# Kernel tuning notes

Hardware: AMD Instinct MI355X
Metric: run time of the kernel (lower is better)

Reference implementation:

```python
import jax, jax.numpy as jnp
import numpy as np

B, T, D, R = 8, 4096, 768, 16
DB = D // 3  # bucket size (d_img = d_sym = 256, d_rf = D - 2*DB = 256)


def setup_inputs() -> dict:
    key = jax.random.key(0)
    ks = jax.random.split(key, 10)
    s = 0.05
    x = jax.random.normal(ks[0], (B, T, D), dtype=jnp.float32)
    # torch nn.Linear stores weight as (out, in); y = x @ W.T + b
    V_w = jax.random.normal(ks[1], (R, D), dtype=jnp.float32) * s
    U_w = jax.random.normal(ks[2], (D, R), dtype=jnp.float32) * s
    E1_w = jax.random.normal(ks[3], (DB, D), dtype=jnp.float32) * s
    E1_b = jnp.zeros((DB,), dtype=jnp.float32)
    E2_w = jax.random.normal(ks[4], (3, DB), dtype=jnp.float32) * s
    E2_b = jnp.zeros((3,), dtype=jnp.float32)
    # a_base init per bucket: img=-0.6, sym=-1.0, rf=-1.6; a_delta init 0 (perturbed so tanh path is exercised)
    a_base = jnp.concatenate([
        jnp.full((DB,), -0.6, dtype=jnp.float32),
        jnp.full((DB,), -1.0, dtype=jnp.float32),
        jnp.full((D - 2 * DB,), -1.6, dtype=jnp.float32),
    ])
    a_delta = jax.random.normal(ks[5], (D,), dtype=jnp.float32) * 0.1
    C_w = jax.random.normal(ks[6], (D, D), dtype=jnp.float32) * s
    G_w = jax.random.normal(ks[7], (D, D), dtype=jnp.float32) * s
    G_b = jnp.zeros((D,), dtype=jnp.float32)
    return {"x": x, "V_w": V_w, "U_w": U_w, "E1_w": E1_w, "E1_b": E1_b,
            "E2_w": E2_w, "E2_b": E2_b, "a_base": a_base, "a_delta": a_delta,
            "C_w": C_w, "G_w": G_w, "G_b": G_b}


def reference(x, V_w, U_w, E1_w, E1_b, E2_w, E2_b, a_base, a_delta, C_w, G_w, G_b):
    d = x.shape[-1]
    db = d // 3
    # Low-rank input projection: Bu = U(V(x))
    Z = jnp.einsum('btd,rd->btr', x, V_w)            # (B,T,R)
    Bu = jnp.einsum('btr,dr->btd', Z, U_w)           # (B,T,D)
    # Evidence scores per timestep (3 clinical buckets)
    h = jax.nn.gelu(jnp.einsum('btd,ed->bte', x, E1_w) + E1_b, approximate=False)
    alpha = jax.nn.sigmoid(jnp.einsum('bte,ce->btc', h, E2_w) + E2_b)  # (B,T,3)
    # Broadcast each bucket's evidence score over its channels
    alpha_rep = jnp.concatenate([
        jnp.broadcast_to(alpha[..., 0:1], alpha.shape[:-1] + (db,)),
        jnp.broadcast_to(alpha[..., 1:2], alpha.shape[:-1] + (db,)),
        jnp.broadcast_to(alpha[..., 2:3], alpha.shape[:-1] + (d - 2 * db,)),
    ], axis=-1)                                       # (B,T,D)
    a_eff = a_base + alpha_rep * jnp.tanh(a_delta)    # (B,T,D)
    lam = jnp.exp(-jax.nn.softplus(-a_eff))           # (B,T,D), in (0,1)
    # Diagonal linear recurrence s_t = lam_t * s_{t-1} + Bu_t  (scan over time)
    def step(s, inp):
        l_t, bu_t = inp
        s = l_t * s + bu_t
        return s, s
    s0 = jnp.zeros(x.shape[:1] + x.shape[2:], dtype=x.dtype)  # (B,D)
    _, S = jax.lax.scan(step, s0, (jnp.swapaxes(lam, 0, 1), jnp.swapaxes(Bu, 0, 1)))
    S = jnp.swapaxes(S, 0, 1)                         # (B,T,D)
    y = jnp.einsum('btd,od->bto', S, C_w)
    gate = jax.nn.sigmoid(jnp.einsum('btd,od->bto', x, G_w) + G_b)
    y = jax.nn.gelu(y, approximate=False) * gate
    return x + y  # dropout is identity in eval mode
```

## Files before the change

kernel.cpp:

```cpp
#include <hip/hip_runtime.h>
#include <hip/hip_bf16.h>
#include <math.h>

#define B_   8
#define T_   4096
#define D_   768
#define R_   16
#define DB_  256
#define N_   (B_ * T_)
#define NC_  64
#define L_   (T_ / NC_)
#define NKS_ (D_ / 32)
#define BUF_ 12288

typedef __attribute__((ext_vector_type(8))) short bf16x8;
typedef __attribute__((ext_vector_type(4))) float f32x4;

__device__ __forceinline__ float gelu_exact(float x) {
    return 0.5f * x * (1.0f + erff(x * 0.70710678118654752f));
}
__device__ __forceinline__ float sigmoidf_(float x) {
    return 1.0f / (1.0f + expf(-x));
}
__device__ __forceinline__ float bf2f(unsigned short u) {
    return __uint_as_float(((unsigned)u) << 16);
}
__device__ __forceinline__ unsigned short f2bf(float f) {
    __hip_bfloat16 h = __float2bfloat16(f);
    return *(unsigned short*)&h;
}
__device__ __forceinline__ bf16x8 pack8(float4 a, float4 b) {
    bf16x8 r;
    r[0] = (short)f2bf(a.x); r[1] = (short)f2bf(a.y);
    r[2] = (short)f2bf(a.z); r[3] = (short)f2bf(a.w);
    r[4] = (short)f2bf(b.x); r[5] = (short)f2bf(b.y);
    r[6] = (short)f2bf(b.z); r[7] = (short)f2bf(b.w);
    return r;
}

__device__ __forceinline__ void gload16(const unsigned short* g, unsigned short* l) {
    __builtin_amdgcn_global_load_lds(
        (const __attribute__((address_space(1))) unsigned int*)(const void*)g,
        (__attribute__((address_space(3))) unsigned int*)(void*)l,
        16, 0, 0);
}

__device__ __forceinline__ void stage_a(const unsigned short* src, int row0, int k0,
                                        unsigned short* lds, int w, int l) {
#pragma unroll
    for (int j = 0; j < 2; ++j) {
        int i   = ((w * 2 + j) << 6) + l;
        int row = i >> 2;
        int q   = i & 3;
        int qs  = q ^ ((row >> 1) & 3);
        gload16(src + (size_t)(row0 + row) * D_ + k0 + qs * 8, lds + ((w * 2 + j) << 9));
    }
}
__device__ __forceinline__ void stage_b(const unsigned short* src, int col0, int k0,
                                        unsigned short* lds, int w, int l) {
    int i   = (w << 6) + l;
    int row = i >> 2;
    int q   = i & 3;
    int qs  = q ^ ((row >> 1) & 3);
    gload16(src + (size_t)(col0 + row) * D_ + k0 + qs * 8, lds + (w << 9));
}

__device__ __forceinline__ bf16x8 frag_read(const unsigned short* lds, int row, int lq) {
    int q = lq ^ ((row >> 1) & 3);
    return *(const bf16x8*)(lds + row * 32 + q * 8);
}

__device__ __forceinline__ void tile_mfma(const unsigned short* la, const unsigned short* lb,
                                          int wrow, int wcol, int lr, int lq,
                                          f32x4 acc[4][4]) {
    bf16x8 a[4], b[4];
#pragma unroll
    for (int m = 0; m < 4; m++) a[m] = frag_read(la, wrow + m * 16 + lr, lq);
#pragma unroll
    for (int n = 0; n < 4; n++) b[n] = frag_read(lb, wcol + n * 16 + lr, lq);
    __builtin_amdgcn_s_setprio(1);
#pragma unroll
    for (int m = 0; m < 4; m++)
#pragma unroll
        for (int n = 0; n < 4; n++)
            acc[m][n] = __builtin_amdgcn_mfma_f32_16x16x32_bf16(a[m], b[n], acc[m][n], 0, 0, 0);
    __builtin_amdgcn_s_setprio(0);
}

__device__ __forceinline__ void kloop_prologue(const unsigned short* __restrict__ A,
                                               const unsigned short* __restrict__ Bm,
                                               int row0, int col0,
                                               unsigned short* lds, int w, int l) {
    stage_a(A, row0, 0,  lds,                w, l);
    stage_b(Bm, col0, 0,  lds + 8192,        w, l);
    stage_a(A, row0, 32, lds + BUF_,         w, l);
    stage_b(Bm, col0, 32, lds + BUF_ + 8192, w, l);
}

template <bool DO_PROLOGUE>
__device__ __forceinline__ void kloop3(const unsigned short* __restrict__ A,
                                       const unsigned short* __restrict__ Bm,
                                       int row0, int col0,
                                       unsigned short* lds,
                                       int w, int l, f32x4 acc[4][4]) {
    const int lr = l & 15, lq = l >> 4;
    const int wrow = (w >> 1) * 64, wcol = (w & 1) * 64;

    if (DO_PROLOGUE) kloop_prologue(A, Bm, row0, col0, lds, w, l);

#pragma unroll 3
    for (int t = 0; t < NKS_ - 2; ++t) {
        asm volatile("s_waitcnt vmcnt(3)" ::: "memory");
        __builtin_amdgcn_s_barrier();
        __builtin_amdgcn_sched_barrier(0);
        unsigned short* bn = lds + ((t + 2) % 3) * BUF_;
        stage_a(A, row0, (t + 2) * 32, bn,        w, l);
        stage_b(Bm, col0, (t + 2) * 32, bn + 8192, w, l);
        unsigned short* bc = lds + (t % 3) * BUF_;
        tile_mfma(bc, bc + 8192, wrow, wcol, lr, lq, acc);
    }
    asm volatile("s_waitcnt vmcnt(3)" ::: "memory");
    __builtin_amdgcn_s_barrier();
    __builtin_amdgcn_sched_barrier(0);
    {
        unsigned short* bc = lds + ((NKS_ - 2) % 3) * BUF_;
        tile_mfma(bc, bc + 8192, wrow, wcol, lr, lq, acc);
    }
    asm volatile("s_waitcnt vmcnt(0)" ::: "memory");
    __builtin_amdgcn_s_barrier();
    __builtin_amdgcn_sched_barrier(0);
    {
        unsigned short* bc = lds + ((NKS_ - 1) % 3) * BUF_;
        tile_mfma(bc, bc + 8192, wrow, wcol, lr, lq, acc);
    }
}

__device__ __forceinline__ void tile_decode(int nwg, int ncol, int& rowt, int& colt) {
    int bid = blockIdx.x;
    int cpx = nwg >> 3;
    int swz = (bid & 7) * cpx + (bid >> 3);
    colt = swz % ncol;
    rowt = swz / ncol;
}

__global__ __launch_bounds__(512, 2)
void gemm_e1_alpha(const unsigned short* __restrict__ Xb,
                   const unsigned short* __restrict__ Wb,
                   const float* __restrict__ bias,
                   const float* __restrict__ E2w,
                   float* __restrict__ alpha_acc) {
    __shared__ unsigned short lds[3 * BUF_];
    const int t = threadIdx.x, l = t & 63, w = t >> 6;
    int rowt, colt;
    tile_decode(256, 2, rowt, colt);
    const int row0 = rowt * 256, col0 = colt * 128;
    const int lr = l & 15, lq = l >> 4;
    const int wrow = (w >> 1) * 64, wcol = (w & 1) * 64;
    f32x4 acc[4][4] = {};
    kloop3<true>(Xb, Wb, row0, col0, lds, w, l, acc);

    float bia[4], e2v[3][4];
#pragma unroll
    for (int n = 0; n < 4; n++) {
        int col = col0 + wcol + n * 16 + lr;
        bia[n] = bias[col];
#pragma unroll
        for (int c = 0; c < 3; c++) e2v[c][n] = E2w[c * DB_ + col];
    }
#pragma unroll
    for (int m = 0; m < 4; m++)
#pragma unroll
        for (int r = 0; r < 4; r++) {
            float p0 = 0.f, p1 = 0.f, p2 = 0.f;
#pragma unroll
            for (int n = 0; n < 4; n++) {
                float h = gelu_exact(acc[m][n][r] + bia[n]);
                p0 = fmaf(h, e2v[0][n], p0);
                p1 = fmaf(h, e2v[1][n], p1);
                p2 = fmaf(h, e2v[2][n], p2);
            }
#pragma unroll
            for (int s = 1; s < 16; s <<= 1) {
                p0 += __shfl_xor(p0, s);
                p1 += __shfl_xor(p1, s);
                p2 += __shfl_xor(p2, s);
            }
            if (lr == 0) {
                int row = row0 + wrow + m * 16 + lq * 4 + r;
                atomicAdd(&alpha_acc[(size_t)row * 3 + 0], p0);
                atomicAdd(&alpha_acc[(size_t)row * 3 + 1], p1);
                atomicAdd(&alpha_acc[(size_t)row * 3 + 2], p2);
            }
        }
}

__global__ __launch_bounds__(512, 2)
void gemm_fused_out(const unsigned short* __restrict__ Xb,
                    const unsigned short* __restrict__ Gwb,
                    const unsigned short* __restrict__ Sb,
                    const unsigned short* __restrict__ Cwb,
                    const float* __restrict__ Gbias,
                    float* __restrict__ out) {
    __shared__ unsigned short lds[3 * BUF_];
    const int t = threadIdx.x, l = t & 63, w = t >> 6;
    int rowt, colt;
    tile_decode(768, 6, rowt, colt);
    const int row0 = rowt * 256, col0 = colt * 128;
    const int lr = l & 15, lq = l >> 4;
    const int wrow = (w >> 1) * 64, wcol = (w & 1) * 64;

    float gb[4];
#pragma unroll
    for (int n = 0; n < 4; n++) gb[n] = Gbias[col0 + wcol + n * 16 + lr];

    f32x4 acc[4][4] = {};
    kloop3<true>(Xb, Gwb, row0, col0, lds, w, l, acc);

    kloop_prologue(Sb, Cwb, row0, col0, lds, w, l);

    unsigned int gp[4][4][2];
#pragma unroll
    for (int m = 0; m < 4; m++)
#pragma unroll
        for (int n = 0; n < 4; n++) {
            gp[m][n][0] = (unsigned)f2bf(sigmoidf_(acc[m][n][0] + gb[n]))
                        | ((unsigned)f2bf(sigmoidf_(acc[m][n][1] + gb[n])) << 16);
            gp[m][n][1] = (unsigned)f2bf(sigmoidf_(acc[m][n][2] + gb[n]))
                        | ((unsigned)f2bf(sigmoidf_(acc[m][n][3] + gb[n])) << 16);
            acc[m][n] = (f32x4){0.f, 0.f, 0.f, 0.f};
        }

    kloop3<false>(Sb, Cwb, row0, col0, lds, w, l, acc);

#pragma unroll
    for (int m = 0; m < 4; m++)
#pragma unroll
        for (int n = 0; n < 4; n++) {
            int col = col0 + wcol + n * 16 + lr;
#pragma unroll
            for (int r = 0; r < 4; r++) {
                int row = row0 + wrow + m * 16 + lq * 4 + r;
                size_t o = (size_t)row * D_ + col;
                float g = bf2f((unsigned short)(gp[m][n][r >> 1] >> ((r & 1) * 16)));
                out[o] = bf2f(Xb[o]) + gelu_exact(acc[m][n][r]) * g;
            }
        }
}

__global__ __launch_bounds__(256)
void cvtz_kernel(const float* __restrict__ X, const float* __restrict__ Vw,
                 unsigned short* __restrict__ Xb, float* __restrict__ Z) {
    const int t = threadIdx.x, l = t & 63, w = t >> 6;
    const int lr = l & 15, lq = l >> 4;
    const int tok0 = (blockIdx.x * 4 + w) * 16;
    const float* xrow = X  + (size_t)(tok0 + lr) * D_;
    const float* vrow = Vw + (size_t)lr * D_;
    f32x4 acc = {};
#pragma unroll 4
    for (int k0 = 0; k0 < D_; k0 += 32) {
        int k = k0 + lq * 8;
        float4 xa = *(const float4*)&xrow[k];
        float4 xb = *(const float4*)&xrow[k + 4];
        float4 va = *(const float4*)&vrow[k];
        float4 vb = *(const float4*)&vrow[k + 4];
        bf16x8 xf = pack8(xa, xb);
        bf16x8 vf = pack8(va, vb);
        *(bf16x8*)&Xb[(size_t)(tok0 + lr) * D_ + k] = xf;
        acc = __builtin_amdgcn_mfma_f32_16x16x32_bf16(xf, vf, acc, 0, 0, 0);
    }
#pragma unroll
    for (int rr = 0; rr < 4; rr++)
        Z[(size_t)(tok0 + lq * 4 + rr) * R_ + lr] = acc[rr];
}

__global__ void zero_f32(float* __restrict__ p, int n) {
    int i = blockIdx.x * 256 + threadIdx.x;
    if (i < n) p[i] = 0.f;
}
__global__ void alpha_fin(const float* __restrict__ acc, const float* __restrict__ E2b,
                          float* __restrict__ alpha, int n) {
    int i = blockIdx.x * 256 + threadIdx.x;
    if (i < n) alpha[i] = sigmoidf_(acc[i] + E2b[i % 3]);
}

__device__ __forceinline__ void load_chunk_lds(const float* __restrict__ Z,
                                               const float* __restrict__ alpha,
                                               int tok0, int t,
                                               float* Zs, float* als) {
#pragma unroll
    for (int i = t; i < L_ * R_ / 4; i += 192)
        *(float4*)&Zs[i * 4] = *(const float4*)&Z[(size_t)tok0 * R_ + i * 4];
    als[t] = alpha[(size_t)tok0 * 3 + t];
}

__device__ __forceinline__ float dot16(const float* zrow, const float4* u) {
    float4 z0 = *(const float4*)&zrow[0],  z1 = *(const float4*)&zrow[4];
    float4 z2 = *(const float4*)&zrow[8],  z3 = *(const float4*)&zrow[12];
    return z0.x*u[0].x + z0.y*u[0].y + z0.z*u[0].z + z0.w*u[0].w
         + z1.x*u[1].x + z1.y*u[1].y + z1.z*u[1].z + z1.w*u[1].w
         + z2.x*u[2].x + z2.y*u[2].y + z2.z*u[2].z + z2.w*u[2].w
         + z3.x*u[3].x + z3.y*u[3].y + z3.z*u[3].z + z3.w*u[3].w;
}

__global__ __launch_bounds__(192)
void scan_pass1(const float* __restrict__ Z, const float* __restrict__ alpha,
                const float* __restrict__ Uw, const float* __restrict__ a_base,
                const float* __restrict__ tanhd,
                float* __restrict__ Aagg, float* __restrict__ Send) {
    __shared__ float Zs[L_ * R_];
    __shared__ float als[L_ * 3];
    const int t = threadIdx.x;
    const int c = blockIdx.x & (NC_ - 1);
    const int b = blockIdx.x >> 6;
    const int tok0 = b * T_ + c * L_;
    const int d0 = t * 4;
    const int buck = d0 >> 8;
    load_chunk_lds(Z, alpha, tok0, t, Zs, als);

    float4 u[4][4];
#pragma unroll
    for (int j = 0; j < 4; j++)
#pragma unroll
        for (int q = 0; q < 4; q++)
            u[j][q] = *(const float4*)&Uw[(size_t)(d0 + j) * R_ + q * 4];
    float4 ab = *(const float4*)&a_base[d0];
    float4 td = *(const float4*)&tanhd[d0];
    float abv[4] = {ab.x, ab.y, ab.z, ab.w};
    float tdv[4] = {td.x, td.y, td.z, td.w};
    __syncthreads();

    float a[4] = {1.f, 1.f, 1.f, 1.f}, s[4] = {};
    for (int i = 0; i < L_; i++) {
        float av = als[i * 3 + buck];
#pragma unroll
        for (int j = 0; j < 4; j++) {
            float lam = sigmoidf_(fmaf(av, tdv[j], abv[j]));
            float bu  = dot16(&Zs[i * R_], u[j]);
            a[j] *= lam;
            s[j] = fmaf(lam, s[j], bu);
        }
    }
    size_t o = ((size_t)(b * NC_ + c)) * D_ + d0;
    *(float4*)&Aagg[o] = make_float4(a[0], a[1], a[2], a[3]);
    *(float4*)&Send[o] = make_float4(s[0], s[1], s[2], s[3]);
}

__global__ void scan_pass2(const float* __restrict__ Aagg, const float* __restrict__ Send,
                           float* __restrict__ Cin) {
    const int d = threadIdx.x;
    const int b = blockIdx.x;
    float s = 0.f;
    for (int c = 0; c < NC_; c++) {
        size_t o = ((size_t)(b * NC_ + c)) * D_ + d;
        Cin[o] = s;
        s = fmaf(Aagg[o], s, Send[o]);
    }
}

__global__ __launch_bounds__(192)
void scan_pass3(const float* __restrict__ Z, const float* __restrict__ alpha,
                const float* __restrict__ Uw, const float* __restrict__ a_base,
                const float* __restrict__ tanhd, const float* __restrict__ Cin,
                unsigned short* __restrict__ Sout) {
    __shared__ float Zs[L_ * R_];
    __shared__ float als[L_ * 3];
    const int t = threadIdx.x;
    const int c = blockIdx.x & (NC_ - 1);
    const int b = blockIdx.x >> 6;
    const int tok0 = b * T_ + c * L_;
    const int d0 = t * 4;
    const int buck = d0 >> 8;
    load_chunk_lds(Z, alpha, tok0, t, Zs, als);

    float4 u[4][4];
#pragma unroll
    for (int j = 0; j < 4; j++)
#pragma unroll
        for (int q = 0; q < 4; q++)
            u[j][q] = *(const float4*)&Uw[(size_t)(d0 + j) * R_ + q * 4];
    float4 ab = *(const float4*)&a_base[d0];
    float4 td = *(const float4*)&tanhd[d0];
    float abv[4] = {ab.x, ab.y, ab.z, ab.w};
    float tdv[4] = {td.x, td.y, td.z, td.w};
    __syncthreads();

    size_t ci = ((size_t)(b * NC_ + c)) * D_ + d0;
    float4 c4 = *(const float4*)&Cin[ci];
    float s[4] = {c4.x, c4.y, c4.z, c4.w};
    for (int i = 0; i < L_; i++) {
        float av = als[i * 3 + buck];
#pragma unroll
        for (int j = 0; j < 4; j++) {
            float lam = sigmoidf_(fmaf(av, tdv[j], abv[j]));
            float bu  = dot16(&Zs[i * R_], u[j]);
            s[j] = fmaf(lam, s[j], bu);
        }
        *(ushort4*)&Sout[(size_t)(tok0 + i) * D_ + d0] =
            make_ushort4(f2bf(s[0]), f2bf(s[1]), f2bf(s[2]), f2bf(s[3]));
    }
}

__global__ void cvt_bf16_vec(const float* __restrict__ in, unsigned short* __restrict__ out, int n4) {
    int i = blockIdx.x * 256 + threadIdx.x;
    if (i < n4) {
        float4 v = ((const float4*)in)[i];
        ((ushort4*)out)[i] = make_ushort4(f2bf(v.x), f2bf(v.y), f2bf(v.z), f2bf(v.w));
    }
}
__global__ void tanh_vec(const float* __restrict__ in, float* __restrict__ out, int n) {
    int i = blockIdx.x * 256 + threadIdx.x;
    if (i < n) out[i] = tanhf(in[i]);
}

extern "C" void kernel_launch(void* const* d_in, const int* in_sizes, int n_in,
                              void* d_out, int out_size, void* d_ws, size_t ws_size,
                              hipStream_t stream) {
    const float* x       = (const float*)d_in[0];
    const float* V_w     = (const float*)d_in[1];
    const float* U_w     = (const float*)d_in[2];
    const float* E1_w    = (const float*)d_in[3];
    const float* E1_b    = (const float*)d_in[4];
    const float* E2_w    = (const float*)d_in[5];
    const float* E2_b    = (const float*)d_in[6];
    const float* a_base  = (const float*)d_in[7];
    const float* a_delta = (const float*)d_in[8];
    const float* C_w     = (const float*)d_in[9];
    const float* G_w     = (const float*)d_in[10];
    const float* G_b     = (const float*)d_in[11];
    float* out = (float*)d_out;

    char* p = (char*)d_ws;
    float* Aagg   = (float*)p;          p += (size_t)B_ * NC_ * D_ * 4;
    float* Send   = (float*)p;          p += (size_t)B_ * NC_ * D_ * 4;
    float* Cin    = (float*)p;          p += (size_t)B_ * NC_ * D_ * 4;
    float* tanhd  = (float*)p;          p += (size_t)D_ * 4;
    float* Z      = (float*)p;          p += (size_t)N_ * R_ * 4;
    float* alpha  = (float*)p;          p += (size_t)N_ * 3 * 4;
    float* al_acc = (float*)p;          p += (size_t)N_ * 3 * 4;
    unsigned short* x_bf  = (unsigned short*)p; p += (size_t)N_ * D_ * 2;
    unsigned short* S_bf  = (unsigned short*)p; p += (size_t)N_ * D_ * 2;
    unsigned short* E1_bf = (unsigned short*)p; p += (size_t)DB_ * D_ * 2;
    unsigned short* Cw_bf = (unsigned short*)p; p += (size_t)D_ * D_ * 2;
    unsigned short* Gw_bf = (unsigned short*)p; p += (size_t)D_ * D_ * 2;

    {
        int n4 = DB_ * D_ / 4;
        cvt_bf16_vec<<<(n4 + 255) / 256, 256, 0, stream>>>(E1_w, E1_bf, n4);
        n4 = D_ * D_ / 4;
        cvt_bf16_vec<<<(n4 + 255) / 256, 256, 0, stream>>>(C_w, Cw_bf, n4);
        cvt_bf16_vec<<<(n4 + 255) / 256, 256, 0, stream>>>(G_w, Gw_bf, n4);
        tanh_vec<<<3, 256, 0, stream>>>(a_delta, tanhd, D_);
        zero_f32<<<(N_ * 3 + 255) / 256, 256, 0, stream>>>(al_acc, N_ * 3);
    }

    cvtz_kernel<<<N_ / 64, 256, 0, stream>>>(x, V_w, x_bf, Z);

    gemm_e1_alpha<<<256, 512, 0, stream>>>(x_bf, E1_bf, E1_b, E2_w, al_acc);
    alpha_fin<<<(N_ * 3 + 255) / 256, 256, 0, stream>>>(al_acc, E2_b, alpha, N_ * 3);

    scan_pass1<<<B_ * NC_, 192, 0, stream>>>(Z, alpha, U_w, a_base, tanhd, Aagg, Send);
    scan_pass2<<<B_,       D_,  0, stream>>>(Aagg, Send, Cin);
    scan_pass3<<<B_ * NC_, 192, 0, stream>>>(Z, alpha, U_w, a_base, tanhd, Cin, S_bf);

    gemm_fused_out<<<768, 512, 0, stream>>>(x_bf, Gw_bf, S_bf, Cw_bf, G_b, out);
}
```

Measured before the change: 301.6 us.

## Retile GEMMs to 4-wave blocks with 8-row-fragment waves and fold alpha sigmoid into scans

Both GEMM kernels move from 512-thread blocks with 2x2 wave tiles to 256-thread blocks. Each wave now covers all 128 rows, 8 M-fragments by NB N-fragments, and reads one A fragment at a time. The E1 GEMM uses 128x128 tiles with 512 blocks, and the fused output GEMM uses 128x256 tiles. LDS buffers and waitcnt values are resized to match. The separate alpha_fin kernel is removed, and the sigmoid plus bias is applied when the scan kernels load alpha, which drops one launch and one intermediate buffer at the cost of recomputing the sigmoid in both scan passes. Register pressure from acc[8][4] plus gp[8][4][2] in the output GEMM is a risk.

```diff
diff --git a/kernel.cpp b/kernel.cpp
--- a/kernel.cpp
+++ b/kernel.cpp
@@ -11,7 +11,6 @@
 #define NC_  64
 #define L_   (T_ / NC_)
 #define NKS_ (D_ / 32)
-#define BUF_ 12288
 
 typedef __attribute__((ext_vector_type(8))) short bf16x8;
 typedef __attribute__((ext_vector_type(4))) float f32x4;
@@ -45,24 +44,26 @@
         16, 0, 0);
 }
 
-__device__ __forceinline__ void stage_a(const unsigned short* src, int row0, int k0,
-                                        unsigned short* lds, int w, int l) {
+template <int NB>
+__device__ __forceinline__ void stage_ab(const unsigned short* __restrict__ A,
+                                         const unsigned short* __restrict__ Bm,
+                                         int row0, int col0, int k0,
+                                         unsigned short* buf, int w, int l) {
 #pragma unroll
     for (int j = 0; j < 2; ++j) {
-        int i   = ((w * 2 + j) << 6) + l;
-        int row = i >> 2;
-        int q   = i & 3;
-        int qs  = q ^ ((row >> 1) & 3);
-        gload16(src + (size_t)(row0 + row) * D_ + k0 + qs * 8, lds + ((w * 2 + j) << 9));
-    }
-}
-__device__ __forceinline__ void stage_b(const unsigned short* src, int col0, int k0,
-                                        unsigned short* lds, int w, int l) {
-    int i   = (w << 6) + l;
-    int row = i >> 2;
-    int q   = i & 3;
-    int qs  = q ^ ((row >> 1) & 3);
-    gload16(src + (size_t)(col0 + row) * D_ + k0 + qs * 8, lds + (w << 9));
+        int i = ((w * 2 + j) << 6) + l;
+        int row = i >> 2, q = i & 3;
+        int qs = q ^ ((row >> 1) & 3);
+        gload16(A + (size_t)(row0 + row) * D_ + k0 + qs * 8, buf + ((w * 2 + j) << 9));
+    }
+    unsigned short* bl = buf + 4096;
+#pragma unroll
+    for (int j = 0; j < NB; ++j) {
+        int i = ((w * NB + j) << 6) + l;
+        int row = i >> 2, q = i & 3;
+        int qs = q ^ ((row >> 1) & 3);
+        gload16(Bm + (size_t)(col0 + row) * D_ + k0 + qs * 8, bl + ((w * NB + j) << 9));
+    }
 }
 
 __device__ __forceinline__ bf16x8 frag_read(const unsigned short* lds, int row, int lq) {
@@ -70,69 +71,66 @@
     return *(const bf16x8*)(lds + row * 32 + q * 8);
 }
 
-__device__ __forceinline__ void tile_mfma(const unsigned short* la, const unsigned short* lb,
-                                          int wrow, int wcol, int lr, int lq,
-                                          f32x4 acc[4][4]) {
-    bf16x8 a[4], b[4];
-#pragma unroll
-    for (int m = 0; m < 4; m++) a[m] = frag_read(la, wrow + m * 16 + lr, lq);
-#pragma unroll
-    for (int n = 0; n < 4; n++) b[n] = frag_read(lb, wcol + n * 16 + lr, lq);
+template <int NB>
+__device__ __forceinline__ void tile_mfma(const unsigned short* buf,
+                                          int wcol, int lr, int lq,
+                                          f32x4 acc[8][NB]) {
+    const unsigned short* la = buf;
+    const unsigned short* lb = buf + 4096;
+    bf16x8 b[NB];
+#pragma unroll
+    for (int n = 0; n < NB; n++) b[n] = frag_read(lb, wcol + n * 16 + lr, lq);
     __builtin_amdgcn_s_setprio(1);
 #pragma unroll
-    for (int m = 0; m < 4; m++)
-#pragma unroll
-        for (int n = 0; n < 4; n++)
-            acc[m][n] = __builtin_amdgcn_mfma_f32_16x16x32_bf16(a[m], b[n], acc[m][n], 0, 0, 0);
+    for (int m = 0; m < 8; m++) {
+        bf16x8 a = frag_read(la, m * 16 + lr, lq);
+#pragma unroll
+        for (int n = 0; n < NB; n++)
+            acc[m][n] = __builtin_amdgcn_mfma_f32_16x16x32_bf16(a, b[n], acc[m][n], 0, 0, 0);
+    }
     __builtin_amdgcn_s_setprio(0);
 }
 
+template <int NB>
 __device__ __forceinline__ void kloop_prologue(const unsigned short* __restrict__ A,
                                                const unsigned short* __restrict__ Bm,
                                                int row0, int col0,
                                                unsigned short* lds, int w, int l) {
-    stage_a(A, row0, 0,  lds,                w, l);
-    stage_b(Bm, col0, 0,  lds + 8192,        w, l);
-    stage_a(A, row0, 32, lds + BUF_,         w, l);
-    stage_b(Bm, col0, 32, lds + BUF_ + 8192, w, l);
-}
-
-template <bool DO_PROLOGUE>
+    constexpr int BUFE = 4096 + NB * 2048;
+    stage_ab<NB>(A, Bm, row0, col0, 0,  lds,        w, l);
+    stage_ab<NB>(A, Bm, row0, col0, 32, lds + BUFE, w, l);
+}
+
+template <int NB, bool DO_PROLOGUE>
 __device__ __forceinline__ void kloop3(const unsigned short* __restrict__ A,
                                        const unsigned short* __restrict__ Bm,
                                        int row0, int col0,
                                        unsigned short* lds,
-                                       int w, int l, f32x4 acc[4][4]) {
+                                       int w, int l, f32x4 acc[8][NB]) {
     const int lr = l & 15, lq = l >> 4;
-    const int wrow = (w >> 1) * 64, wcol = (w & 1) * 64;
-
-    if (DO_PROLOGUE) kloop_prologue(A, Bm, row0, col0, lds, w, l);
+    const int wcol = w * NB * 16;
+    constexpr int BUFE = 4096 + NB * 2048;
+
+    if (DO_PROLOGUE) kloop_prologue<NB>(A, Bm, row0, col0, lds, w, l);
 
 #pragma unroll 3
     for (int t = 0; t < NKS_ - 2; ++t) {
-        asm volatile("s_waitcnt vmcnt(3)" ::: "memory");
+        if constexpr (NB == 4) asm volatile("s_waitcnt vmcnt(6)" ::: "memory");
+        else                   asm volatile("s_waitcnt vmcnt(4)" ::: "memory");
         __builtin_amdgcn_s_barrier();
         __builtin_amdgcn_sched_barrier(0);
-        unsigned short* bn = lds + ((t + 2) % 3) * BUF_;
-        stage_a(A, row0, (t + 2) * 32, bn,        w, l);
-        stage_b(Bm, col0, (t + 2) * 32, bn + 8192, w, l);
-        unsigned short* bc = lds + (t % 3) * BUF_;
-        tile_mfma(bc, bc + 8192, wrow, wcol, lr, lq, acc);
-    }
-    asm volatile("s_waitcnt vmcnt(3)" ::: "memory");
+        stage_ab<NB>(A, Bm, row0, col0, (t + 2) * 32, lds + ((t + 2) % 3) * BUFE, w, l);
+        tile_mfma<NB>(lds + (t % 3) * BUFE, wcol, lr, lq, acc);
+    }
+    if constexpr (NB == 4) asm volatile("s_waitcnt vmcnt(6)" ::: "memory");
+    else                   asm volatile("s_waitcnt vmcnt(4)" ::: "memory");
     __builtin_amdgcn_s_barrier();
     __builtin_amdgcn_sched_barrier(0);
-    {
-        unsigned short* bc = lds + ((NKS_ - 2) % 3) * BUF_;
-        tile_mfma(bc, bc + 8192, wrow, wcol, lr, lq, acc);
-    }
+    tile_mfma<NB>(lds + ((NKS_ - 2) % 3) * BUFE, wcol, lr, lq, acc);
     asm volatile("s_waitcnt vmcnt(0)" ::: "memory");
     __builtin_amdgcn_s_barrier();
     __builtin_amdgcn_sched_barrier(0);
-    {
-        unsigned short* bc = lds + ((NKS_ - 1) % 3) * BUF_;
-        tile_mfma(bc, bc + 8192, wrow, wcol, lr, lq, acc);
-    }
+    tile_mfma<NB>(lds + ((NKS_ - 1) % 3) * BUFE, wcol, lr, lq, acc);
 }
 
 __device__ __forceinline__ void tile_decode(int nwg, int ncol, int& rowt, int& colt) {
@@ -143,37 +141,37 @@
     rowt = swz / ncol;
 }
 
-__global__ __launch_bounds__(512, 2)
+__global__ __launch_bounds__(256, 3)
 void gemm_e1_alpha(const unsigned short* __restrict__ Xb,
                    const unsigned short* __restrict__ Wb,
                    const float* __restrict__ bias,
                    const float* __restrict__ E2w,
                    float* __restrict__ alpha_acc) {
-    __shared__ unsigned short lds[3 * BUF_];
+    __shared__ unsigned short lds[3 * (4096 + 2 * 2048)];
     const int t = threadIdx.x, l = t & 63, w = t >> 6;
     int rowt, colt;
-    tile_decode(256, 2, rowt, colt);
-    const int row0 = rowt * 256, col0 = colt * 128;
+    tile_decode(512, 2, rowt, colt);
+    const int row0 = rowt * 128, col0 = colt * 128;
     const int lr = l & 15, lq = l >> 4;
-    const int wrow = (w >> 1) * 64, wcol = (w & 1) * 64;
-    f32x4 acc[4][4] = {};
-    kloop3<true>(Xb, Wb, row0, col0, lds, w, l, acc);
-
-    float bia[4], e2v[3][4];
-#pragma unroll
-    for (int n = 0; n < 4; n++) {
+    const int wcol = w * 32;
+    f32x4 acc[8][2] = {};
+    kloop3<2, true>(Xb, Wb, row0, col0, lds, w, l, acc);
+
+    float bia[2], e2v[3][2];
+#pragma unroll
+    for (int n = 0; n < 2; n++) {
         int col = col0 + wcol + n * 16 + lr;
         bia[n] = bias[col];
 #pragma unroll
         for (int c = 0; c < 3; c++) e2v[c][n] = E2w[c * DB_ + col];
     }
 #pragma unroll
-    for (int m = 0; m < 4; m++)
+    for (int m = 0; m < 8; m++)
 #pragma unroll
         for (int r = 0; r < 4; r++) {
             float p0 = 0.f, p1 = 0.f, p2 = 0.f;
 #pragma unroll
-            for (int n = 0; n < 4; n++) {
+            for (int n = 0; n < 2; n++) {
                 float h = gelu_exact(acc[m][n][r] + bia[n]);
                 p0 = fmaf(h, e2v[0][n], p0);
                 p1 = fmaf(h, e2v[1][n], p1);
@@ -186,7 +184,7 @@
                 p2 += __shfl_xor(p2, s);
             }
             if (lr == 0) {
-                int row = row0 + wrow + m * 16 + lq * 4 + r;
+                int row = row0 + m * 16 + lq * 4 + r;
                 atomicAdd(&alpha_acc[(size_t)row * 3 + 0], p0);
                 atomicAdd(&alpha_acc[(size_t)row * 3 + 1], p1);
                 atomicAdd(&alpha_acc[(size_t)row * 3 + 2], p2);
@@ -194,33 +192,33 @@
         }
 }
 
-__global__ __launch_bounds__(512, 2)
+__global__ __launch_bounds__(256, 2)
 void gemm_fused_out(const unsigned short* __restrict__ Xb,
                     const unsigned short* __restrict__ Gwb,
                     const unsigned short* __restrict__ Sb,
                     const unsigned short* __restrict__ Cwb,
                     const float* __restrict__ Gbias,
                     float* __restrict__ out) {
-    __shared__ unsigned short lds[3 * BUF_];
+    __shared__ unsigned short lds[3 * (4096 + 4 * 2048)];
     const int t = threadIdx.x, l = t & 63, w = t >> 6;
     int rowt, colt;
-    tile_decode(768, 6, rowt, colt);
-    const int row0 = rowt * 256, col0 = colt * 128;
+    tile_decode(768, 3, rowt, colt);
+    const int row0 = rowt * 128, col0 = colt * 256;
     const int lr = l & 15, lq = l >> 4;
-    const int wrow = (w >> 1) * 64, wcol = (w & 1) * 64;
+    const int wcol = w * 64;
 
     float gb[4];
 #pragma unroll
     for (int n = 0; n < 4; n++) gb[n] = Gbias[col0 + wcol + n * 16 + lr];
 
-    f32x4 acc[4][4] = {};
-    kloop3<true>(Xb, Gwb, row0, col0, lds, w, l, acc);
-
-    kloop_prologue(Sb, Cwb, row0, col0, lds, w, l);
-
-    unsigned int gp[4][4][2];
-#pragma unroll
-    for (int m = 0; m < 4; m++)
+    f32x4 acc[8][4] = {};
+    kloop3<4, true>(Xb, Gwb, row0, col0, lds, w, l, acc);
+
+    kloop_prologue<4>(Sb, Cwb, row0, col0, lds, w, l);
+
+    unsigned int gp[8][4][2];
+#pragma unroll
+    for (int m = 0; m < 8; m++)
 #pragma unroll
         for (int n = 0; n < 4; n++) {
             gp[m][n][0] = (unsigned)f2bf(sigmoidf_(acc[m][n][0] + gb[n]))
@@ -230,16 +228,16 @@
             acc[m][n] = (f32x4){0.f, 0.f, 0.f, 0.f};
         }
 
-    kloop3<false>(Sb, Cwb, row0, col0, lds, w, l, acc);
-
-#pragma unroll
-    for (int m = 0; m < 4; m++)
+    kloop3<4, false>(Sb, Cwb, row0, col0, lds, w, l, acc);
+
+#pragma unroll
+    for (int m = 0; m < 8; m++)
 #pragma unroll
         for (int n = 0; n < 4; n++) {
             int col = col0 + wcol + n * 16 + lr;
 #pragma unroll
             for (int r = 0; r < 4; r++) {
-                int row = row0 + wrow + m * 16 + lq * 4 + r;
+                int row = row0 + m * 16 + lq * 4 + r;
                 size_t o = (size_t)row * D_ + col;
                 float g = bf2f((unsigned short)(gp[m][n][r >> 1] >> ((r & 1) * 16)));
                 out[o] = bf2f(Xb[o]) + gelu_exact(acc[m][n][r]) * g;
@@ -277,20 +275,16 @@
     int i = blockIdx.x * 256 + threadIdx.x;
     if (i < n) p[i] = 0.f;
 }
-__global__ void alpha_fin(const float* __restrict__ acc, const float* __restrict__ E2b,
-                          float* __restrict__ alpha, int n) {
-    int i = blockIdx.x * 256 + threadIdx.x;
-    if (i < n) alpha[i] = sigmoidf_(acc[i] + E2b[i % 3]);
-}
 
 __device__ __forceinline__ void load_chunk_lds(const float* __restrict__ Z,
-                                               const float* __restrict__ alpha,
+                                               const float* __restrict__ al_acc,
+                                               const float* __restrict__ E2b,
                                                int tok0, int t,
                                                float* Zs, float* als) {
 #pragma unroll
     for (int i = t; i < L_ * R_ / 4; i += 192)
         *(float4*)&Zs[i * 4] = *(const float4*)&Z[(size_t)tok0 * R_ + i * 4];
-    als[t] = alpha[(size_t)tok0 * 3 + t];
+    als[t] = sigmoidf_(al_acc[(size_t)tok0 * 3 + t] + E2b[t % 3]);
 }
 
 __device__ __forceinline__ float dot16(const float* zrow, const float4* u) {
@@ -303,7 +297,8 @@
 }
 
 __global__ __launch_bounds__(192)
-void scan_pass1(const float* __restrict__ Z, const float* __restrict__ alpha,
+void scan_pass1(const float* __restrict__ Z, const float* __restrict__ al_acc,
+                const float* __restrict__ E2b,
                 const float* __restrict__ Uw, const float* __restrict__ a_base,
                 const float* __restrict__ tanhd,
                 float* __restrict__ Aagg, float* __restrict__ Send) {
@@ -315,7 +310,7 @@
     const int tok0 = b * T_ + c * L_;
     const int d0 = t * 4;
     const int buck = d0 >> 8;
-    load_chunk_lds(Z, alpha, tok0, t, Zs, als);
+    load_chunk_lds(Z, al_acc, E2b, tok0, t, Zs, als);
 
     float4 u[4][4];
 #pragma unroll
@@ -358,7 +353,8 @@
 }
 
 __global__ __launch_bounds__(192)
-void scan_pass3(const float* __restrict__ Z, const float* __restrict__ alpha,
+void scan_pass3(const float* __restrict__ Z, const float* __restrict__ al_acc,
+                const float* __restrict__ E2b,
                 const float* __restrict__ Uw, const float* __restrict__ a_base,
                 const float* __restrict__ tanhd, const float* __restrict__ Cin,
                 unsigned short* __restrict__ Sout) {
@@ -370,7 +366,7 @@
     const int tok0 = b * T_ + c * L_;
     const int d0 = t * 4;
     const int buck = d0 >> 8;
-    load_chunk_lds(Z, alpha, tok0, t, Zs, als);
+    load_chunk_lds(Z, al_acc, E2b, tok0, t, Zs, als);
 
     float4 u[4][4];
 #pragma unroll
@@ -435,7 +431,6 @@
     float* Cin    = (float*)p;          p += (size_t)B_ * NC_ * D_ * 4;
     float* tanhd  = (float*)p;          p += (size_t)D_ * 4;
     float* Z      = (float*)p;          p += (size_t)N_ * R_ * 4;
-    float* alpha  = (float*)p;          p += (size_t)N_ * 3 * 4;
     float* al_acc = (float*)p;          p += (size_t)N_ * 3 * 4;
     unsigned short* x_bf  = (unsigned short*)p; p += (size_t)N_ * D_ * 2;
     unsigned short* S_bf  = (unsigned short*)p; p += (size_t)N_ * D_ * 2;
@@ -455,12 +450,11 @@
 
     cvtz_kernel<<<N_ / 64, 256, 0, stream>>>(x, V_w, x_bf, Z);
 
-    gemm_e1_alpha<<<256, 512, 0, stream>>>(x_bf, E1_bf, E1_b, E2_w, al_acc);
-    alpha_fin<<<(N_ * 3 + 255) / 256, 256, 0, stream>>>(al_acc, E2_b, alpha, N_ * 3);
-
-    scan_pass1<<<B_ * NC_, 192, 0, stream>>>(Z, alpha, U_w, a_base, tanhd, Aagg, Send);
+    gemm_e1_alpha<<<512, 256, 0, stream>>>(x_bf, E1_bf, E1_b, E2_w, al_acc);
+
+    scan_pass1<<<B_ * NC_, 192, 0, stream>>>(Z, al_acc, E2_b, U_w, a_base, tanhd, Aagg, Send);
     scan_pass2<<<B_,       D_,  0, stream>>>(Aagg, Send, Cin);
-    scan_pass3<<<B_ * NC_, 192, 0, stream>>>(Z, alpha, U_w, a_base, tanhd, Cin, S_bf);
-
-    gemm_fused_out<<<768, 512, 0, stream>>>(x_bf, Gw_bf, S_bf, Cw_bf, G_b, out);
-}
+    scan_pass3<<<B_ * NC_, 192, 0, stream>>>(Z, al_acc, E2_b, U_w, a_base, tanhd, Cin, S_bf);
+
+    gemm_fused_out<<<768, 256, 0, stream>>>(x_bf, Gw_bf, S_bf, Cw_bf, G_b, out);
+}
```

Result: slower. 404.1 us (+34.0%).

## Widen output GEMM tiles to 256x256 and fuse setup and alpha-finalize kernels

Applied to the files above, without the earlier changes.

The fused output GEMM moves from 256x128 to 256x256 tiles with 8x4 MFMA accumulators per wave, using 384 workgroups at one block per CU. This cuts redundant A-operand loads and raises MFMA work per LDS read, at the cost of more registers and lower occupancy. Five small setup kernels are merged into one launch, and the alpha sigmoid finalize is folded into the scan kernels' chunk loads, which removes launches and an intermediate buffer.

```diff
diff --git a/kernel.cpp b/kernel.cpp
--- a/kernel.cpp
+++ b/kernel.cpp
@@ -11,7 +11,8 @@
 #define NC_  64
 #define L_   (T_ / NC_)
 #define NKS_ (D_ / 32)
-#define BUF_ 12288
+#define BUF_  12288
+#define BUF2_ 16384
 
 typedef __attribute__((ext_vector_type(8))) short bf16x8;
 typedef __attribute__((ext_vector_type(4))) float f32x4;
@@ -45,34 +46,40 @@
         16, 0, 0);
 }
 
-__device__ __forceinline__ void stage_a(const unsigned short* src, int row0, int k0,
-                                        unsigned short* lds, int w, int l) {
-#pragma unroll
-    for (int j = 0; j < 2; ++j) {
-        int i   = ((w * 2 + j) << 6) + l;
-        int row = i >> 2;
-        int q   = i & 3;
-        int qs  = q ^ ((row >> 1) & 3);
-        gload16(src + (size_t)(row0 + row) * D_ + k0 + qs * 8, lds + ((w * 2 + j) << 9));
-    }
-}
-__device__ __forceinline__ void stage_b(const unsigned short* src, int col0, int k0,
-                                        unsigned short* lds, int w, int l) {
-    int i   = (w << 6) + l;
-    int row = i >> 2;
-    int q   = i & 3;
-    int qs  = q ^ ((row >> 1) & 3);
-    gload16(src + (size_t)(col0 + row) * D_ + k0 + qs * 8, lds + (w << 9));
-}
-
 __device__ __forceinline__ bf16x8 frag_read(const unsigned short* lds, int row, int lq) {
     int q = lq ^ ((row >> 1) & 3);
     return *(const bf16x8*)(lds + row * 32 + q * 8);
 }
 
-__device__ __forceinline__ void tile_mfma(const unsigned short* la, const unsigned short* lb,
-                                          int wrow, int wcol, int lr, int lq,
-                                          f32x4 acc[4][4]) {
+__device__ __forceinline__ void tile_decode(int nwg, int ncol, int& rowt, int& colt) {
+    int bid = blockIdx.x;
+    int cpx = nwg >> 3;
+    int swz = (bid & 7) * cpx + (bid >> 3);
+    colt = swz % ncol;
+    rowt = swz / ncol;
+}
+
+__device__ __forceinline__ void stage_a(const unsigned short* src, int row0, int k0,
+                                        unsigned short* lds, int w, int l) {
+#pragma unroll
+    for (int j = 0; j < 2; ++j) {
+        int i = ((w * 2 + j) << 6) + l;
+        int row = i >> 2, q = i & 3;
+        int qs = q ^ ((row >> 1) & 3);
+        gload16(src + (size_t)(row0 + row) * D_ + k0 + qs * 8, lds + ((w * 2 + j) << 9));
+    }
+}
+__device__ __forceinline__ void stage_b(const unsigned short* src, int col0, int k0,
+                                        unsigned short* lds, int w, int l) {
+    int i = (w << 6) + l;
+    int row = i >> 2, q = i & 3;
+    int qs = q ^ ((row >> 1) & 3);
+    gload16(src + (size_t)(col0 + row) * D_ + k0 + qs * 8, lds + (w << 9));
+}
+
+__device__ __forceinline__ void tile_mfma44(const unsigned short* la, const unsigned short* lb,
+                                            int wrow, int wcol, int lr, int lq,
+                                            f32x4 acc[4][4]) {
     bf16x8 a[4], b[4];
 #pragma unroll
     for (int m = 0; m < 4; m++) a[m] = frag_read(la, wrow + m * 16 + lr, lq);
@@ -87,26 +94,18 @@
     __builtin_amdgcn_s_setprio(0);
 }
 
-__device__ __forceinline__ void kloop_prologue(const unsigned short* __restrict__ A,
-                                               const unsigned short* __restrict__ Bm,
-                                               int row0, int col0,
-                                               unsigned short* lds, int w, int l) {
-    stage_a(A, row0, 0,  lds,                w, l);
-    stage_b(Bm, col0, 0,  lds + 8192,        w, l);
-    stage_a(A, row0, 32, lds + BUF_,         w, l);
-    stage_b(Bm, col0, 32, lds + BUF_ + 8192, w, l);
-}
-
-template <bool DO_PROLOGUE>
-__device__ __forceinline__ void kloop3(const unsigned short* __restrict__ A,
-                                       const unsigned short* __restrict__ Bm,
-                                       int row0, int col0,
-                                       unsigned short* lds,
-                                       int w, int l, f32x4 acc[4][4]) {
+__device__ __forceinline__ void kloop3_128(const unsigned short* __restrict__ A,
+                                           const unsigned short* __restrict__ Bm,
+                                           int row0, int col0,
+                                           unsigned short* lds,
+                                           int w, int l, f32x4 acc[4][4]) {
     const int lr = l & 15, lq = l >> 4;
     const int wrow = (w >> 1) * 64, wcol = (w & 1) * 64;
 
-    if (DO_PROLOGUE) kloop_prologue(A, Bm, row0, col0, lds, w, l);
+    stage_a(A,  row0, 0,  lds,                w, l);
+    stage_b(Bm, col0, 0,  lds + 8192,         w, l);
+    stage_a(A,  row0, 32, lds + BUF_,         w, l);
+    stage_b(Bm, col0, 32, lds + BUF_ + 8192,  w, l);
 
 #pragma unroll 3
     for (int t = 0; t < NKS_ - 2; ++t) {
@@ -114,33 +113,102 @@
         __builtin_amdgcn_s_barrier();
         __builtin_amdgcn_sched_barrier(0);
         unsigned short* bn = lds + ((t + 2) % 3) * BUF_;
-        stage_a(A, row0, (t + 2) * 32, bn,        w, l);
+        stage_a(A,  row0, (t + 2) * 32, bn,        w, l);
         stage_b(Bm, col0, (t + 2) * 32, bn + 8192, w, l);
         unsigned short* bc = lds + (t % 3) * BUF_;
-        tile_mfma(bc, bc + 8192, wrow, wcol, lr, lq, acc);
+        tile_mfma44(bc, bc + 8192, wrow, wcol, lr, lq, acc);
     }
     asm volatile("s_waitcnt vmcnt(3)" ::: "memory");
     __builtin_amdgcn_s_barrier();
     __builtin_amdgcn_sched_barrier(0);
     {
         unsigned short* bc = lds + ((NKS_ - 2) % 3) * BUF_;
-        tile_mfma(bc, bc + 8192, wrow, wcol, lr, lq, acc);
+        tile_mfma44(bc, bc + 8192, wrow, wcol, lr, lq, acc);
     }
     asm volatile("s_waitcnt vmcnt(0)" ::: "memory");
     __builtin_amdgcn_s_barrier();
     __builtin_amdgcn_sched_barrier(0);
     {
         unsigned short* bc = lds + ((NKS_ - 1) % 3) * BUF_;
-        tile_mfma(bc, bc + 8192, wrow, wcol, lr, lq, acc);
-    }
-}
-
-__device__ __forceinline__ void tile_decode(int nwg, int ncol, int& rowt, int& colt) {
-    int bid = blockIdx.x;
-    int cpx = nwg >> 3;
-    int swz = (bid & 7) * cpx + (bid >> 3);
-    colt = swz % ncol;
-    rowt = swz / ncol;
+        tile_mfma44(bc, bc + 8192, wrow, wcol, lr, lq, acc);
+    }
+}
+
+__device__ __forceinline__ void stage_ab256(const unsigned short* __restrict__ A,
+                                            const unsigned short* __restrict__ Bm,
+                                            int row0, int col0, int k0,
+                                            unsigned short* buf, int w, int l) {
+#pragma unroll
+    for (int j = 0; j < 2; ++j) {
+        int i = ((w * 2 + j) << 6) + l;
+        int row = i >> 2, q = i & 3;
+        int qs = q ^ ((row >> 1) & 3);
+        gload16(A + (size_t)(row0 + row) * D_ + k0 + qs * 8, buf + ((w * 2 + j) << 9));
+    }
+    unsigned short* bl = buf + 8192;
+#pragma unroll
+    for (int j = 0; j < 2; ++j) {
+        int i = ((w * 2 + j) << 6) + l;
+        int row = i >> 2, q = i & 3;
+        int qs = q ^ ((row >> 1) & 3);
+        gload16(Bm + (size_t)(col0 + row) * D_ + k0 + qs * 8, bl + ((w * 2 + j) << 9));
+    }
+}
+
+__device__ __forceinline__ void tile_mfma84(const unsigned short* buf,
+                                            int wrow, int wcol, int lr, int lq,
+                                            f32x4 acc[8][4]) {
+    const unsigned short* la = buf;
+    const unsigned short* lb = buf + 8192;
+    bf16x8 b[4];
+#pragma unroll
+    for (int n = 0; n < 4; n++) b[n] = frag_read(lb, wcol + n * 16 + lr, lq);
+    __builtin_amdgcn_s_setprio(1);
+#pragma unroll
+    for (int m = 0; m < 8; m++) {
+        bf16x8 a = frag_read(la, wrow + m * 16 + lr, lq);
+#pragma unroll
+        for (int n = 0; n < 4; n++)
+            acc[m][n] = __builtin_amdgcn_mfma_f32_16x16x32_bf16(a, b[n], acc[m][n], 0, 0, 0);
+    }
+    __builtin_amdgcn_s_setprio(0);
+}
+
+__device__ __forceinline__ void prologue256(const unsigned short* __restrict__ A,
+                                            const unsigned short* __restrict__ Bm,
+                                            int row0, int col0,
+                                            unsigned short* lds, int w, int l) {
+    stage_ab256(A, Bm, row0, col0, 0,  lds,         w, l);
+    stage_ab256(A, Bm, row0, col0, 32, lds + BUF2_, w, l);
+}
+
+template <bool DO_PROLOGUE>
+__device__ __forceinline__ void kloop3_256(const unsigned short* __restrict__ A,
+                                           const unsigned short* __restrict__ Bm,
+                                           int row0, int col0,
+                                           unsigned short* lds,
+                                           int w, int l, f32x4 acc[8][4]) {
+    const int lr = l & 15, lq = l >> 4;
+    const int wrow = (w >> 2) * 128, wcol = (w & 3) * 64;
+
+    if (DO_PROLOGUE) prologue256(A, Bm, row0, col0, lds, w, l);
+
+#pragma unroll 3
+    for (int t = 0; t < NKS_ - 2; ++t) {
+        asm volatile("s_waitcnt vmcnt(4)" ::: "memory");
+        __builtin_amdgcn_s_barrier();
+        __builtin_amdgcn_sched_barrier(0);
+        stage_ab256(A, Bm, row0, col0, (t + 2) * 32, lds + ((t + 2) % 3) * BUF2_, w, l);
+        tile_mfma84(lds + (t % 3) * BUF2_, wrow, wcol, lr, lq, acc);
+    }
+    asm volatile("s_waitcnt vmcnt(4)" ::: "memory");
+    __builtin_amdgcn_s_barrier();
+    __builtin_amdgcn_sched_barrier(0);
+    tile_mfma84(lds + ((NKS_ - 2) % 3) * BUF2_, wrow, wcol, lr, lq, acc);
+    asm volatile("s_waitcnt vmcnt(0)" ::: "memory");
+    __builtin_amdgcn_s_barrier();
+    __builtin_amdgcn_sched_barrier(0);
+    tile_mfma84(lds + ((NKS_ - 1) % 3) * BUF2_, wrow, wcol, lr, lq, acc);
 }
 
 __global__ __launch_bounds__(512, 2)
@@ -157,7 +225,7 @@
     const int lr = l & 15, lq = l >> 4;
     const int wrow = (w >> 1) * 64, wcol = (w & 1) * 64;
     f32x4 acc[4][4] = {};
-    kloop3<true>(Xb, Wb, row0, col0, lds, w, l, acc);
+    kloop3_128(Xb, Wb, row0, col0, lds, w, l, acc);
 
     float bia[4], e2v[3][4];
 #pragma unroll
@@ -194,33 +262,33 @@
         }
 }
 
-__global__ __launch_bounds__(512, 2)
+__global__ __launch_bounds__(512, 1)
 void gemm_fused_out(const unsigned short* __restrict__ Xb,
                     const unsigned short* __restrict__ Gwb,
                     const unsigned short* __restrict__ Sb,
                     const unsigned short* __restrict__ Cwb,
                     const float* __restrict__ Gbias,
                     float* __restrict__ out) {
-    __shared__ unsigned short lds[3 * BUF_];
+    __shared__ unsigned short lds[3 * BUF2_];
     const int t = threadIdx.x, l = t & 63, w = t >> 6;
     int rowt, colt;
-    tile_decode(768, 6, rowt, colt);
-    const int row0 = rowt * 256, col0 = colt * 128;
+    tile_decode(384, 3, rowt, colt);
+    const int row0 = rowt * 256, col0 = colt * 256;
     const int lr = l & 15, lq = l >> 4;
-    const int wrow = (w >> 1) * 64, wcol = (w & 1) * 64;
+    const int wrow = (w >> 2) * 128, wcol = (w & 3) * 64;
 
     float gb[4];
 #pragma unroll
     for (int n = 0; n < 4; n++) gb[n] = Gbias[col0 + wcol + n * 16 + lr];
 
-    f32x4 acc[4][4] = {};
-    kloop3<true>(Xb, Gwb, row0, col0, lds, w, l, acc);
-
-    kloop_prologue(Sb, Cwb, row0, col0, lds, w, l);
-
-    unsigned int gp[4][4][2];
-#pragma unroll
-    for (int m = 0; m < 4; m++)
+    f32x4 acc[8][4] = {};
+    kloop3_256<true>(Xb, Gwb, row0, col0, lds, w, l, acc);
+
+    prologue256(Sb, Cwb, row0, col0, lds, w, l);
+
+    unsigned int gp[8][4][2];
+#pragma unroll
+    for (int m = 0; m < 8; m++)
 #pragma unroll
         for (int n = 0; n < 4; n++) {
             gp[m][n][0] = (unsigned)f2bf(sigmoidf_(acc[m][n][0] + gb[n]))
@@ -230,10 +298,10 @@
             acc[m][n] = (f32x4){0.f, 0.f, 0.f, 0.f};
         }
 
-    kloop3<false>(Sb, Cwb, row0, col0, lds, w, l, acc);
-
-#pragma unroll
-    for (int m = 0; m < 4; m++)
+    kloop3_256<false>(Sb, Cwb, row0, col0, lds, w, l, acc);
+
+#pragma unroll
+    for (int m = 0; m < 8; m++)
 #pragma unroll
         for (int n = 0; n < 4; n++) {
             int col = col0 + wcol + n * 16 + lr;
@@ -273,24 +341,49 @@
         Z[(size_t)(tok0 + lq * 4 + rr) * R_ + lr] = acc[rr];
 }
 
-__global__ void zero_f32(float* __restrict__ p, int n) {
+#define SEG_E1  (DB_ * D_ / 4)
+#define SEG_W   (D_ * D_ / 4)
+#define SEG_Z   (N_ * 3 / 4)
+#define SEG_TOT (SEG_E1 + 2 * SEG_W + SEG_Z + 192)
+
+__global__ void setup_all(const float* __restrict__ E1_w, const float* __restrict__ C_w,
+                          const float* __restrict__ G_w, const float* __restrict__ a_delta,
+                          unsigned short* __restrict__ E1b, unsigned short* __restrict__ Cwb,
+                          unsigned short* __restrict__ Gwb, float* __restrict__ al_acc,
+                          float* __restrict__ tanhd) {
     int i = blockIdx.x * 256 + threadIdx.x;
-    if (i < n) p[i] = 0.f;
-}
-__global__ void alpha_fin(const float* __restrict__ acc, const float* __restrict__ E2b,
-                          float* __restrict__ alpha, int n) {
-    int i = blockIdx.x * 256 + threadIdx.x;
-    if (i < n) alpha[i] = sigmoidf_(acc[i] + E2b[i % 3]);
+    if (i < SEG_E1) {
+        float4 v = ((const float4*)E1_w)[i];
+        ((ushort4*)E1b)[i] = make_ushort4(f2bf(v.x), f2bf(v.y), f2bf(v.z), f2bf(v.w));
+    } else if (i < SEG_E1 + SEG_W) {
+        int j = i - SEG_E1;
+        float4 v = ((const float4*)C_w)[j];
+        ((ushort4*)Cwb)[j] = make_ushort4(f2bf(v.x), f2bf(v.y), f2bf(v.z), f2bf(v.w));
+    } else if (i < SEG_E1 + 2 * SEG_W) {
+        int j = i - SEG_E1 - SEG_W;
+        float4 v = ((const float4*)G_w)[j];
+        ((ushort4*)Gwb)[j] = make_ushort4(f2bf(v.x), f2bf(v.y), f2bf(v.z), f2bf(v.w));
+    } else if (i < SEG_E1 + 2 * SEG_W + SEG_Z) {
+        int j = i - SEG_E1 - 2 * SEG_W;
+        ((float4*)al_acc)[j] = make_float4(0.f, 0.f, 0.f, 0.f);
+    } else if (i < SEG_TOT) {
+        int j = (i - SEG_E1 - 2 * SEG_W - SEG_Z) * 4;
+        tanhd[j + 0] = tanhf(a_delta[j + 0]);
+        tanhd[j + 1] = tanhf(a_delta[j + 1]);
+        tanhd[j + 2] = tanhf(a_delta[j + 2]);
+        tanhd[j + 3] = tanhf(a_delta[j + 3]);
+    }
 }
 
 __device__ __forceinline__ void load_chunk_lds(const float* __restrict__ Z,
-                                               const float* __restrict__ alpha,
+                                               const float* __restrict__ al_acc,
+                                               const float* __restrict__ E2b,
                                                int tok0, int t,
                                                float* Zs, float* als) {
 #pragma unroll
     for (int i = t; i < L_ * R_ / 4; i += 192)
         *(float4*)&Zs[i * 4] = *(const float4*)&Z[(size_t)tok0 * R_ + i * 4];
-    als[t] = alpha[(size_t)tok0 * 3 + t];
+    als[t] = sigmoidf_(al_acc[(size_t)tok0 * 3 + t] + E2b[t % 3]);
 }
 
 __device__ __forceinline__ float dot16(const float* zrow, const float4* u) {
@@ -303,7 +396,8 @@
 }
 
 __global__ __launch_bounds__(192)
-void scan_pass1(const float* __restrict__ Z, const float* __restrict__ alpha,
+void scan_pass1(const float* __restrict__ Z, const float* __restrict__ al_acc,
+                const float* __restrict__ E2b,
                 const float* __restrict__ Uw, const float* __restrict__ a_base,
                 const float* __restrict__ tanhd,
                 float* __restrict__ Aagg, float* __restrict__ Send) {
@@ -315,7 +409,7 @@
     const int tok0 = b * T_ + c * L_;
     const int d0 = t * 4;
     const int buck = d0 >> 8;
-    load_chunk_lds(Z, alpha, tok0, t, Zs, als);
+    load_chunk_lds(Z, al_acc, E2b, tok0, t, Zs, als);
 
     float4 u[4][4];
 #pragma unroll
@@ -358,7 +452,8 @@
 }
 
 __global__ __launch_bounds__(192)
-void scan_pass3(const float* __restrict__ Z, const float* __restrict__ alpha,
+void scan_pass3(const float* __restrict__ Z, const float* __restrict__ al_acc,
+                const float* __restrict__ E2b,
                 const float* __restrict__ Uw, const float* __restrict__ a_base,
                 const float* __restrict__ tanhd, const float* __restrict__ Cin,
                 unsigned short* __restrict__ Sout) {
@@ -370,7 +465,7 @@
     const int tok0 = b * T_ + c * L_;
     const int d0 = t * 4;
     const int buck = d0 >> 8;
-    load_chunk_lds(Z, alpha, tok0, t, Zs, als);
+    load_chunk_lds(Z, al_acc, E2b, tok0, t, Zs, als);
 
     float4 u[4][4];
 #pragma unroll
@@ -398,18 +493,6 @@
         *(ushort4*)&Sout[(size_t)(tok0 + i) * D_ + d0] =
             make_ushort4(f2bf(s[0]), f2bf(s[1]), f2bf(s[2]), f2bf(s[3]));
     }
-}
-
-__global__ void cvt_bf16_vec(const float* __restrict__ in, unsigned short* __restrict__ out, int n4) {
-    int i = blockIdx.x * 256 + threadIdx.x;
-    if (i < n4) {
-        float4 v = ((const float4*)in)[i];
-        ((ushort4*)out)[i] = make_ushort4(f2bf(v.x), f2bf(v.y), f2bf(v.z), f2bf(v.w));
-    }
-}
-__global__ void tanh_vec(const float* __restrict__ in, float* __restrict__ out, int n) {
-    int i = blockIdx.x * 256 + threadIdx.x;
-    if (i < n) out[i] = tanhf(in[i]);
 }
 
 extern "C" void kernel_launch(void* const* d_in, const int* in_sizes, int n_in,
@@ -435,7 +518,6 @@
     float* Cin    = (float*)p;          p += (size_t)B_ * NC_ * D_ * 4;
     float* tanhd  = (float*)p;          p += (size_t)D_ * 4;
     float* Z      = (float*)p;          p += (size_t)N_ * R_ * 4;
-    float* alpha  = (float*)p;          p += (size_t)N_ * 3 * 4;
     float* al_acc = (float*)p;          p += (size_t)N_ * 3 * 4;
     unsigned short* x_bf  = (unsigned short*)p; p += (size_t)N_ * D_ * 2;
     unsigned short* S_bf  = (unsigned short*)p; p += (size_t)N_ * D_ * 2;
@@ -443,24 +525,16 @@
     unsigned short* Cw_bf = (unsigned short*)p; p += (size_t)D_ * D_ * 2;
     unsigned short* Gw_bf = (unsigned short*)p; p += (size_t)D_ * D_ * 2;
 
-    {
-        int n4 = DB_ * D_ / 4;
-        cvt_bf16_vec<<<(n4 + 255) / 256, 256, 0, stream>>>(E1_w, E1_bf, n4);
-        n4 = D_ * D_ / 4;
-        cvt_bf16_vec<<<(n4 + 255) / 256, 256, 0, stream>>>(C_w, Cw_bf, n4);
-        cvt_bf16_vec<<<(n4 + 255) / 256, 256, 0, stream>>>(G_w, Gw_bf, n4);
-        tanh_vec<<<3, 256, 0, stream>>>(a_delta, tanhd, D_);
-        zero_f32<<<(N_ * 3 + 255) / 256, 256, 0, stream>>>(al_acc, N_ * 3);
-    }
+    setup_all<<<(SEG_TOT + 255) / 256, 256, 0, stream>>>(
+        E1_w, C_w, G_w, a_delta, E1_bf, Cw_bf, Gw_bf, al_acc, tanhd);
 
     cvtz_kernel<<<N_ / 64, 256, 0, stream>>>(x, V_w, x_bf, Z);
 
     gemm_e1_alpha<<<256, 512, 0, stream>>>(x_bf, E1_bf, E1_b, E2_w, al_acc);
-    alpha_fin<<<(N_ * 3 + 255) / 256, 256, 0, stream>>>(al_acc, E2_b, alpha, N_ * 3);
-
-    scan_pass1<<<B_ * NC_, 192, 0, stream>>>(Z, alpha, U_w, a_base, tanhd, Aagg, Send);
+
+    scan_pass1<<<B_ * NC_, 192, 0, stream>>>(Z, al_acc, E2_b, U_w, a_base, tanhd, Aagg, Send);
     scan_pass2<<<B_,       D_,  0, stream>>>(Aagg, Send, Cin);
-    scan_pass3<<<B_ * NC_, 192, 0, stream>>>(Z, alpha, U_w, a_base, tanhd, Cin, S_bf);
-
-    gemm_fused_out<<<768, 512, 0, stream>>>(x_bf, Gw_bf, S_bf, Cw_bf, G_b, out);
-}
+    scan_pass3<<<B_ * NC_, 192, 0, stream>>>(Z, al_acc, E2_b, U_w, a_base, tanhd, Cin, S_bf);
+
+    gemm_fused_out<<<384, 512, 0, stream>>>(x_bf, Gw_bf, S_bf, Cw_bf, G_b, out);
+}
```

Result: slower. 363.6 us (+20.6%).
